# Kernel tuning notes

Measured on AMD Instinct MI355X. Metric: run time of the kernel, lower is better.

## Reference

```python
import jax, jax.numpy as jnp
import numpy as np

N_NODES = 50000
N_EDGES = 800000
IN_DIM = 4
HID = 64
N_LAYERS = 3
BN_EPS = 1e-5


def setup_inputs() -> dict:
    key = jax.random.key(0)
    ks = jax.random.split(key, 16)
    x = jax.random.normal(ks[0], (N_NODES, IN_DIM), dtype=jnp.float32)
    edge_index = jax.random.randint(ks[1], (2, N_EDGES), 0, N_NODES, dtype=jnp.int32)
    # input projection
    W_in = jax.random.normal(ks[2], (IN_DIM, HID), dtype=jnp.float32) * 0.1
    b_in = jnp.zeros((HID,), dtype=jnp.float32)
    # stacked per-layer GCN weights and BatchNorm (eval-mode) params
    conv_w = jax.random.normal(ks[3], (N_LAYERS, HID, HID), dtype=jnp.float32) * 0.1
    conv_b = jnp.zeros((N_LAYERS, HID), dtype=jnp.float32)
    bn_gamma = jnp.ones((N_LAYERS, HID), dtype=jnp.float32)
    bn_beta = jnp.zeros((N_LAYERS, HID), dtype=jnp.float32)
    bn_mean = jax.random.normal(ks[4], (N_LAYERS, HID), dtype=jnp.float32) * 0.01
    bn_var = jnp.abs(jax.random.normal(ks[5], (N_LAYERS, HID), dtype=jnp.float32)) * 0.1 + 1.0
    # output projection: Linear(HID,HID) -> ReLU -> Dropout(eval: identity) -> Linear(HID,OUT)
    W1 = jax.random.normal(ks[6], (HID, HID), dtype=jnp.float32) * 0.1
    b1 = jnp.zeros((HID,), dtype=jnp.float32)
    W2 = jax.random.normal(ks[7], (HID, IN_DIM), dtype=jnp.float32) * 0.01  # xavier gain 0.1
    b2 = jnp.zeros((IN_DIM,), dtype=jnp.float32)
    return {
        "x": x, "edge_index": edge_index,
        "W_in": W_in, "b_in": b_in,
        "conv_w": conv_w, "conv_b": conv_b,
        "bn_gamma": bn_gamma, "bn_beta": bn_beta,
        "bn_mean": bn_mean, "bn_var": bn_var,
        "W1": W1, "b1": b1, "W2": W2, "b2": b2,
    }


def _gcn_graph(edge_index, n_nodes):
    """Add self loops and compute symmetric GCN normalization per edge."""
    loops = jnp.arange(n_nodes, dtype=edge_index.dtype)
    src = jnp.concatenate([edge_index[0], loops])
    dst = jnp.concatenate([edge_index[1], loops])
    deg = jax.ops.segment_sum(jnp.ones_like(dst, dtype=jnp.float32), dst,
                              num_segments=n_nodes)  # in-degree incl. self loop
    dinv = jax.lax.rsqrt(jnp.maximum(deg, 1e-12))
    enorm = dinv[src] * dinv[dst]  # [E+N]
    return src, dst, enorm


def reference(x, edge_index, W_in, b_in, conv_w, conv_b, bn_gamma, bn_beta,
              bn_mean, bn_var, W1, b1, W2, b2):
    n = x.shape[0]
    src, dst, enorm = _gcn_graph(edge_index, n)

    input_x = x
    h = x @ W_in + b_in  # [N, HID]
    for i in range(N_LAYERS):
        residual = h
        # GCNConv: linear -> normalized gather/scatter aggregate -> bias
        hw = h @ conv_w[i]
        msg = hw[src] * enorm[:, None]  # [E+N, HID] irregular gather
        h = jax.ops.segment_sum(msg, dst, num_segments=n) + conv_b[i]
        # BatchNorm1d (eval) + ReLU (dropout is identity in eval)
        h = (h - bn_mean[i]) * jax.lax.rsqrt(bn_var[i] + BN_EPS) * bn_gamma[i] + bn_beta[i]
        h = jax.nn.relu(h)
        h = h + residual  # shapes always match (HID == HID)
    # output projection MLP
    delta = jax.nn.relu(h @ W1 + b1) @ W2 + b2  # [N, IN_DIM]
    return input_x + delta
```

## Files before the change

### kernel.cpp

```cpp
#include <hip/hip_runtime.h>

#define HID 64
#define CAP 64

__device__ __forceinline__ float bf2f(unsigned short u) {
    return __uint_as_float(((unsigned)u) << 16);
}
__device__ __forceinline__ unsigned short f2bf(float f) {
    unsigned u = __float_as_uint(f);
    u += 0x7FFF + ((u >> 16) & 1);
    return (unsigned short)(u >> 16);
}

__global__ void fill_gemm(const int* __restrict__ eidx, int* __restrict__ cursor,
                          int* __restrict__ col, int E, int n, int nodes_per,
                          int chunk, int fillBlocks,
                          const float* __restrict__ x, const float* __restrict__ Win,
                          const float* __restrict__ bin, const float* __restrict__ W,
                          float* __restrict__ h, unsigned short* __restrict__ hws0) {
    if (blockIdx.x < fillBlocks) {
        int p = blockIdx.x & 7;
        int q = blockIdx.x >> 3;
        const int* __restrict__ dst = eidx + E;
        int lo = p * nodes_per;
        int hi = lo + nodes_per;
        int beg = q * chunk;
        int end = min(beg + chunk, E);
        int vend = beg + ((end - beg) & ~3);
        for (int e = beg + threadIdx.x * 4; e < vend; e += 1024) {
            int4 dv = *(const int4*)&dst[e];
            if (dv.x >= lo && dv.x < hi) {
                int s = eidx[e];
                int pos = atomicAdd(&cursor[dv.x], 1);
                if (pos < CAP) col[(dv.x << 6) + pos] = s;
            }
            if (dv.y >= lo && dv.y < hi) {
                int s = eidx[e + 1];
                int pos = atomicAdd(&cursor[dv.y], 1);
                if (pos < CAP) col[(dv.y << 6) + pos] = s;
            }
            if (dv.z >= lo && dv.z < hi) {
                int s = eidx[e + 2];
                int pos = atomicAdd(&cursor[dv.z], 1);
                if (pos < CAP) col[(dv.z << 6) + pos] = s;
            }
            if (dv.w >= lo && dv.w < hi) {
                int s = eidx[e + 3];
                int pos = atomicAdd(&cursor[dv.w], 1);
                if (pos < CAP) col[(dv.w << 6) + pos] = s;
            }
        }
        for (int e = vend + threadIdx.x; e < end; e += 256) {
            int d = dst[e];
            if (d >= lo && d < hi) {
                int s = eidx[e];
                int pos = atomicAdd(&cursor[d], 1);
                if (pos < CAP) col[(d << 6) + pos] = s;
            }
        }
        return;
    }
    __shared__ float wl[64 * 64];
    __shared__ float winl[256];
    __shared__ float binl[64];
    __shared__ float hl[256];
    int b = blockIdx.x - fillBlocks;
    int tid = threadIdx.x;
#pragma unroll
    for (int i = 0; i < 16; ++i) wl[tid + 256 * i] = W[tid + 256 * i];
    winl[tid] = Win[tid];
    if (tid < 64) binl[tid] = bin[tid];
    int j = tid & 63;
    int w = tid >> 6;
    for (int c = 0; c < 8; ++c) {
        int v = b * 32 + c * 4 + w;
        __syncthreads();
        float hv = 0.f;
        if (v < n) {
            float4 xv = *(const float4*)&x[(size_t)v * 4];
            hv = binl[j] + xv.x * winl[j] + xv.y * winl[64 + j]
                         + xv.z * winl[128 + j] + xv.w * winl[192 + j];
            h[(size_t)v * 64 + j] = hv;
        }
        hl[tid] = hv;
        __syncthreads();
        if (v < n) {
            const float* hr = &hl[w * 64];
            float acc = 0.f;
#pragma unroll
            for (int k = 0; k < 64; ++k) acc += hr[k] * wl[k * 64 + j];
            hws0[(size_t)v * 64 + j] = f2bf(acc);
        }
    }
}

#define GATHER_BODY_D(hws4, col, cur, beg, end, s0, s1, s2, s3, gl)               \
    {                                                                             \
        int e = beg;                                                              \
        for (; e + 7 < end; e += 8) {                                             \
            int c0 = col[e], c1 = col[e+1], c2 = col[e+2], c3 = col[e+3];         \
            int c4 = col[e+4], c5 = col[e+5], c6 = col[e+6], c7 = col[e+7];       \
            float d0 = rsqrtf((float)cur[c0] + 1.0f);                             \
            float d1 = rsqrtf((float)cur[c1] + 1.0f);                             \
            float d2 = rsqrtf((float)cur[c2] + 1.0f);                             \
            float d3 = rsqrtf((float)cur[c3] + 1.0f);                             \
            float d4 = rsqrtf((float)cur[c4] + 1.0f);                             \
            float d5 = rsqrtf((float)cur[c5] + 1.0f);                             \
            float d6 = rsqrtf((float)cur[c6] + 1.0f);                             \
            float d7 = rsqrtf((float)cur[c7] + 1.0f);                             \
            ushort4 m0 = hws4[(size_t)c0 * 16 + gl];                              \
            ushort4 m1 = hws4[(size_t)c1 * 16 + gl];                              \
            ushort4 m2 = hws4[(size_t)c2 * 16 + gl];                              \
            ushort4 m3 = hws4[(size_t)c3 * 16 + gl];                              \
            ushort4 m4 = hws4[(size_t)c4 * 16 + gl];                              \
            ushort4 m5 = hws4[(size_t)c5 * 16 + gl];                              \
            ushort4 m6 = hws4[(size_t)c6 * 16 + gl];                              \
            ushort4 m7 = hws4[(size_t)c7 * 16 + gl];                              \
            s0 = fmaf(bf2f(m0.x), d0, s0); s0 = fmaf(bf2f(m1.x), d1, s0);         \
            s0 = fmaf(bf2f(m2.x), d2, s0); s0 = fmaf(bf2f(m3.x), d3, s0);         \
            s0 = fmaf(bf2f(m4.x), d4, s0); s0 = fmaf(bf2f(m5.x), d5, s0);         \
            s0 = fmaf(bf2f(m6.x), d6, s0); s0 = fmaf(bf2f(m7.x), d7, s0);         \
            s1 = fmaf(bf2f(m0.y), d0, s1); s1 = fmaf(bf2f(m1.y), d1, s1);         \
            s1 = fmaf(bf2f(m2.y), d2, s1); s1 = fmaf(bf2f(m3.y), d3, s1);         \
            s1 = fmaf(bf2f(m4.y), d4, s1); s1 = fmaf(bf2f(m5.y), d5, s1);         \
            s1 = fmaf(bf2f(m6.y), d6, s1); s1 = fmaf(bf2f(m7.y), d7, s1);         \
            s2 = fmaf(bf2f(m0.z), d0, s2); s2 = fmaf(bf2f(m1.z), d1, s2);         \
            s2 = fmaf(bf2f(m2.z), d2, s2); s2 = fmaf(bf2f(m3.z), d3, s2);         \
            s2 = fmaf(bf2f(m4.z), d4, s2); s2 = fmaf(bf2f(m5.z), d5, s2);         \
            s2 = fmaf(bf2f(m6.z), d6, s2); s2 = fmaf(bf2f(m7.z), d7, s2);         \
            s3 = fmaf(bf2f(m0.w), d0, s3); s3 = fmaf(bf2f(m1.w), d1, s3);         \
            s3 = fmaf(bf2f(m2.w), d2, s3); s3 = fmaf(bf2f(m3.w), d3, s3);         \
            s3 = fmaf(bf2f(m4.w), d4, s3); s3 = fmaf(bf2f(m5.w), d5, s3);         \
            s3 = fmaf(bf2f(m6.w), d6, s3); s3 = fmaf(bf2f(m7.w), d7, s3);         \
        }                                                                         \
        for (; e < end; ++e) {                                                    \
            int c0 = col[e];                                                      \
            float d0 = rsqrtf((float)cur[c0] + 1.0f);                             \
            ushort4 me = hws4[(size_t)c0 * 16 + gl];                              \
            s0 = fmaf(bf2f(me.x), d0, s0); s1 = fmaf(bf2f(me.y), d0, s1);         \
            s2 = fmaf(bf2f(me.z), d0, s2); s3 = fmaf(bf2f(me.w), d0, s3);         \
        }                                                                         \
    }

#define GATHER_BODY_P(hws4, col, beg, end, s0, s1, s2, s3, gl)                    \
    {                                                                             \
        int e = beg;                                                              \
        for (; e + 7 < end; e += 8) {                                             \
            int c0 = col[e], c1 = col[e+1], c2 = col[e+2], c3 = col[e+3];         \
            int c4 = col[e+4], c5 = col[e+5], c6 = col[e+6], c7 = col[e+7];       \
            ushort4 m0 = hws4[(size_t)c0 * 16 + gl];                              \
            ushort4 m1 = hws4[(size_t)c1 * 16 + gl];                              \
            ushort4 m2 = hws4[(size_t)c2 * 16 + gl];                              \
            ushort4 m3 = hws4[(size_t)c3 * 16 + gl];                              \
            ushort4 m4 = hws4[(size_t)c4 * 16 + gl];                              \
            ushort4 m5 = hws4[(size_t)c5 * 16 + gl];                              \
            ushort4 m6 = hws4[(size_t)c6 * 16 + gl];                              \
            ushort4 m7 = hws4[(size_t)c7 * 16 + gl];                              \
            s0 += bf2f(m0.x)+bf2f(m1.x)+bf2f(m2.x)+bf2f(m3.x)                     \
                + bf2f(m4.x)+bf2f(m5.x)+bf2f(m6.x)+bf2f(m7.x);                    \
            s1 += bf2f(m0.y)+bf2f(m1.y)+bf2f(m2.y)+bf2f(m3.y)                     \
                + bf2f(m4.y)+bf2f(m5.y)+bf2f(m6.y)+bf2f(m7.y);                    \
            s2 += bf2f(m0.z)+bf2f(m1.z)+bf2f(m2.z)+bf2f(m3.z)                     \
                + bf2f(m4.z)+bf2f(m5.z)+bf2f(m6.z)+bf2f(m7.z);                    \
            s3 += bf2f(m0.w)+bf2f(m1.w)+bf2f(m2.w)+bf2f(m3.w)                     \
                + bf2f(m4.w)+bf2f(m5.w)+bf2f(m6.w)+bf2f(m7.w);                    \
        }                                                                         \
        for (; e + 3 < end; e += 4) {                                             \
            int c0 = col[e], c1 = col[e+1], c2 = col[e+2], c3 = col[e+3];         \
            ushort4 m0 = hws4[(size_t)c0 * 16 + gl];                              \
            ushort4 m1 = hws4[(size_t)c1 * 16 + gl];                              \
            ushort4 m2 = hws4[(size_t)c2 * 16 + gl];                              \
            ushort4 m3 = hws4[(size_t)c3 * 16 + gl];                              \
            s0 += bf2f(m0.x)+bf2f(m1.x)+bf2f(m2.x)+bf2f(m3.x);                    \
            s1 += bf2f(m0.y)+bf2f(m1.y)+bf2f(m2.y)+bf2f(m3.y);                    \
            s2 += bf2f(m0.z)+bf2f(m1.z)+bf2f(m2.z)+bf2f(m3.z);                    \
            s3 += bf2f(m0.w)+bf2f(m1.w)+bf2f(m2.w)+bf2f(m3.w);                    \
        }                                                                         \
        for (; e < end; ++e) {                                                    \
            ushort4 me = hws4[(size_t)col[e] * 16 + gl];                          \
            s0 += bf2f(me.x); s1 += bf2f(me.y); s2 += bf2f(me.z); s3 += bf2f(me.w);\
        }                                                                         \
    }

template <bool PRESCALED>
__global__ void gather_gemm(const int* __restrict__ cursor, const int* __restrict__ col,
                            const unsigned short* __restrict__ hws_in,
                            float* __restrict__ h,
                            const float* __restrict__ cb, const float* __restrict__ gamma,
                            const float* __restrict__ beta, const float* __restrict__ mean,
                            const float* __restrict__ var, const float* __restrict__ Wn,
                            unsigned short* __restrict__ hws_out, int n) {
    __shared__ float wl[64 * 64];
    __shared__ float hl[16 * 64];
    int tid = threadIdx.x;
#pragma unroll
    for (int i = 0; i < 16; ++i) wl[tid + 256 * i] = Wn[tid + 256 * i];
    int lane = tid & 63, wave = tid >> 6;
    int grp = lane >> 4, gl = lane & 15;
    int ln = wave * 4 + grp;
    int v = blockIdx.x * 16 + ln;
    bool valid = v < n;
    int vv = valid ? v : 0;
    int j0 = gl * 4;
    const ushort4* hws4 = (const ushort4*)hws_in;
    int cnt = cursor[vv];
    float di = rsqrtf((float)cnt + 1.0f);
    ushort4 m = hws4[(size_t)vv * 16 + gl];
    float s0, s1, s2, s3;
    if (PRESCALED) {
        s0 = bf2f(m.x); s1 = bf2f(m.y); s2 = bf2f(m.z); s3 = bf2f(m.w);
    } else {
        s0 = bf2f(m.x) * di; s1 = bf2f(m.y) * di;
        s2 = bf2f(m.z) * di; s3 = bf2f(m.w) * di;
    }
    int beg = vv << 6;
    int end = beg + (valid ? min(cnt, CAP) : 0);
    if (PRESCALED) {
        GATHER_BODY_P(hws4, col, beg, end, s0, s1, s2, s3, gl)
    } else {
        GATHER_BODY_D(hws4, col, cursor, beg, end, s0, s1, s2, s3, gl)
    }
    float4 cbv = *(const float4*)&cb[j0];
    float4 mnv = *(const float4*)&mean[j0];
    float4 vrv = *(const float4*)&var[j0];
    float4 gmv = *(const float4*)&gamma[j0];
    float4 btv = *(const float4*)&beta[j0];
    float4 hres = *(const float4*)&h[(size_t)vv * 64 + j0];
    float4 o;
    o.x = fmaxf((s0 * di + cbv.x - mnv.x) * rsqrtf(vrv.x + 1e-5f) * gmv.x + btv.x, 0.f) + hres.x;
    o.y = fmaxf((s1 * di + cbv.y - mnv.y) * rsqrtf(vrv.y + 1e-5f) * gmv.y + btv.y, 0.f) + hres.y;
    o.z = fmaxf((s2 * di + cbv.z - mnv.z) * rsqrtf(vrv.z + 1e-5f) * gmv.z + btv.z, 0.f) + hres.z;
    o.w = fmaxf((s3 * di + cbv.w - mnv.w) * rsqrtf(vrv.w + 1e-5f) * gmv.w + btv.w, 0.f) + hres.w;
    if (valid) *(float4*)&h[(size_t)vv * 64 + j0] = o;
    *(float4*)&hl[ln * 64 + j0] = o;
    __syncthreads();
    int j = lane;
    for (int c = 0; c < 4; ++c) {
        int ln2 = wave * 4 + c;
        int v2 = blockIdx.x * 16 + ln2;
        if (v2 < n) {
            const float* hr = &hl[ln2 * 64];
            float acc = 0.f;
#pragma unroll
            for (int k = 0; k < 64; ++k) acc += hr[k] * wl[k * 64 + j];
            float di2 = rsqrtf((float)cursor[v2] + 1.0f);
            hws_out[(size_t)v2 * 64 + j] = f2bf(acc * di2);
        }
    }
}

__global__ void gather_mlp(const int* __restrict__ cursor, const int* __restrict__ col,
                           const unsigned short* __restrict__ hws_in,
                           const float* __restrict__ h,
                           const float* __restrict__ cb, const float* __restrict__ gamma,
                           const float* __restrict__ beta, const float* __restrict__ mean,
                           const float* __restrict__ var, const float* __restrict__ x,
                           const float* __restrict__ W1, const float* __restrict__ b1,
                           const float* __restrict__ W2, const float* __restrict__ b2,
                           float* __restrict__ out, int n) {
    __shared__ float wl[64 * 64];
    __shared__ float w2l[256];
    __shared__ float hl[16 * 64];
    __shared__ float tl[16 * 68];
    int tid = threadIdx.x;
#pragma unroll
    for (int i = 0; i < 16; ++i) wl[tid + 256 * i] = W1[tid + 256 * i];
    w2l[tid] = W2[tid];
    int lane = tid & 63, wave = tid >> 6;
    int grp = lane >> 4, gl = lane & 15;
    int ln = wave * 4 + grp;
    int v = blockIdx.x * 16 + ln;
    bool valid = v < n;
    int vv = valid ? v : 0;
    int j0 = gl * 4;
    const ushort4* hws4 = (const ushort4*)hws_in;
    int cnt = cursor[vv];
    float di = rsqrtf((float)cnt + 1.0f);
    ushort4 m = hws4[(size_t)vv * 16 + gl];
    float s0 = bf2f(m.x), s1 = bf2f(m.y), s2 = bf2f(m.z), s3 = bf2f(m.w);
    int beg = vv << 6;
    int end = beg + (valid ? min(cnt, CAP) : 0);
    GATHER_BODY_P(hws4, col, beg, end, s0, s1, s2, s3, gl)
    float4 cbv = *(const float4*)&cb[j0];
    float4 mnv = *(const float4*)&mean[j0];
    float4 vrv = *(const float4*)&var[j0];
    float4 gmv = *(const float4*)&gamma[j0];
    float4 btv = *(const float4*)&beta[j0];
    float4 hres = *(const float4*)&h[(size_t)vv * 64 + j0];
    float4 o;
    o.x = fmaxf((s0 * di + cbv.x - mnv.x) * rsqrtf(vrv.x + 1e-5f) * gmv.x + btv.x, 0.f) + hres.x;
    o.y = fmaxf((s1 * di + cbv.y - mnv.y) * rsqrtf(vrv.y + 1e-5f) * gmv.y + btv.y, 0.f) + hres.y;
    o.z = fmaxf((s2 * di + cbv.z - mnv.z) * rsqrtf(vrv.z + 1e-5f) * gmv.z + btv.z, 0.f) + hres.z;
    o.w = fmaxf((s3 * di + cbv.w - mnv.w) * rsqrtf(vrv.w + 1e-5f) * gmv.w + btv.w, 0.f) + hres.w;
    *(float4*)&hl[ln * 64 + j0] = o;
    __syncthreads();
    int j = lane;
    float b1j = b1[j];
    for (int c = 0; c < 4; ++c) {
        int ln2 = wave * 4 + c;
        const float* hr = &hl[ln2 * 64];
        float acc = b1j;
#pragma unroll
        for (int k = 0; k < 64; ++k) acc += hr[k] * wl[k * 64 + j];
        tl[ln2 * 68 + j] = fmaxf(acc, 0.f);
    }
    __syncthreads();
    if (tid < 64) {
        int ln2 = tid >> 2, mm = tid & 3;
        int v2 = blockIdx.x * 16 + ln2;
        if (v2 < n) {
            const float* tr = &tl[ln2 * 68];
            float acc = b2[mm];
#pragma unroll
            for (int k = 0; k < 64; ++k) acc += tr[k] * w2l[k * 4 + mm];
            out[(size_t)v2 * 4 + mm] = x[(size_t)v2 * 4 + mm] + acc;
        }
    }
}

extern "C" void kernel_launch(void* const* d_in, const int* in_sizes, int n_in,
                              void* d_out, int out_size, void* d_ws, size_t ws_size,
                              hipStream_t stream) {
    const float* x     = (const float*)d_in[0];
    const int*   eidx  = (const int*)  d_in[1];
    const float* Win   = (const float*)d_in[2];
    const float* bin   = (const float*)d_in[3];
    const float* convw = (const float*)d_in[4];
    const float* convb = (const float*)d_in[5];
    const float* gamma = (const float*)d_in[6];
    const float* beta  = (const float*)d_in[7];
    const float* mean  = (const float*)d_in[8];
    const float* var   = (const float*)d_in[9];
    const float* W1    = (const float*)d_in[10];
    const float* b1    = (const float*)d_in[11];
    const float* W2    = (const float*)d_in[12];
    const float* b2    = (const float*)d_in[13];
    float* out = (float*)d_out;

    int n = in_sizes[0] / 4;
    int E = in_sizes[1] / 2;
    const int B = 256;

    char* p = (char*)d_ws;
    size_t nh = (size_t)n * 64;
    float*          h      = (float*)p;          p += nh * 4;
    unsigned short* hws0   = (unsigned short*)p; p += nh * 2;
    unsigned short* hws1   = (unsigned short*)p; p += nh * 2;
    int*            cursor = (int*)p;            p += ((size_t)n + 16) * 4;
    int*            col    = (int*)p;            p += (size_t)n * CAP * 4;

    const int GP = 128;
    int fillBlocks = GP * 8;
    int nodes_per = (n + 7) / 8;
    int chunk = (((E + GP - 1) / GP) + 3) & ~3;

    hipMemsetAsync(cursor, 0, (size_t)n * 4, stream);
    int NB32 = (n + 31) / 32;
    fill_gemm<<<fillBlocks + NB32, B, 0, stream>>>(
        eidx, cursor, col, E, n, nodes_per, chunk, fillBlocks,
        x, Win, bin, convw, h, hws0);

    int NB16 = (n + 15) / 16;
    gather_gemm<false><<<NB16, B, 0, stream>>>(cursor, col, hws0, h,
        convb, gamma, beta, mean, var, convw + 4096, hws1, n);
    gather_gemm<true><<<NB16, B, 0, stream>>>(cursor, col, hws1, h,
        convb + 64, gamma + 64, beta + 64, mean + 64, var + 64, convw + 8192, hws0, n);
    gather_mlp<<<NB16, B, 0, stream>>>(cursor, col, hws0, h,
        convb + 128, gamma + 128, beta + 128, mean + 128, var + 128,
        x, W1, b1, W2, b2, out, n);
}
```

Baseline: 235.8 us.

## Split feature gathers into two 32-column halves for L2-resident working sets

The bf16 per-node feature table is stored as two separate 32-column half arrays. Each layer's gather runs as two passes: one kernel gathers the first half into an fp32 scratch buffer, and a second gathers the other half and then applies the epilogue and GEMM. Each pass touches a table half the size, about 3.2MB, so it is meant to fit in cache and cut random-access DRAM traffic. In exchange it adds three kernel launches, reads the col index lists twice per layer, and writes and reads an extra fp32 scratch buffer.

```diff
diff --git a/kernel.cpp b/kernel.cpp
--- a/kernel.cpp
+++ b/kernel.cpp
@@ -1,6 +1,5 @@
 #include <hip/hip_runtime.h>
 
-#define HID 64
 #define CAP 64
 
 __device__ __forceinline__ float bf2f(unsigned short u) {
@@ -17,7 +16,8 @@
                           int chunk, int fillBlocks,
                           const float* __restrict__ x, const float* __restrict__ Win,
                           const float* __restrict__ bin, const float* __restrict__ W,
-                          float* __restrict__ h, unsigned short* __restrict__ hws0) {
+                          float* __restrict__ h, unsigned short* __restrict__ hwsA0,
+                          unsigned short* __restrict__ hwsB0) {
     if (blockIdx.x < fillBlocks) {
         int p = blockIdx.x & 7;
         int q = blockIdx.x >> 3;
@@ -89,12 +89,14 @@
             float acc = 0.f;
 #pragma unroll
             for (int k = 0; k < 64; ++k) acc += hr[k] * wl[k * 64 + j];
-            hws0[(size_t)v * 64 + j] = f2bf(acc);
-        }
-    }
-}
-
-#define GATHER_BODY_D(hws4, col, cur, beg, end, s0, s1, s2, s3, gl)               \
+            unsigned short bb = f2bf(acc);
+            if (j < 32) hwsA0[(size_t)v * 32 + j] = bb;
+            else        hwsB0[(size_t)v * 32 + (j - 32)] = bb;
+        }
+    }
+}
+
+#define GH_D(hws2, col, cur, beg, end, s0, s1, gl)                                \
     {                                                                             \
         int e = beg;                                                              \
         for (; e + 7 < end; e += 8) {                                             \
@@ -108,14 +110,14 @@
             float d5 = rsqrtf((float)cur[c5] + 1.0f);                             \
             float d6 = rsqrtf((float)cur[c6] + 1.0f);                             \
             float d7 = rsqrtf((float)cur[c7] + 1.0f);                             \
-            ushort4 m0 = hws4[(size_t)c0 * 16 + gl];                              \
-            ushort4 m1 = hws4[(size_t)c1 * 16 + gl];                              \
-            ushort4 m2 = hws4[(size_t)c2 * 16 + gl];                              \
-            ushort4 m3 = hws4[(size_t)c3 * 16 + gl];                              \
-            ushort4 m4 = hws4[(size_t)c4 * 16 + gl];                              \
-            ushort4 m5 = hws4[(size_t)c5 * 16 + gl];                              \
-            ushort4 m6 = hws4[(size_t)c6 * 16 + gl];                              \
-            ushort4 m7 = hws4[(size_t)c7 * 16 + gl];                              \
+            ushort2 m0 = hws2[(size_t)c0 * 16 + gl];                              \
+            ushort2 m1 = hws2[(size_t)c1 * 16 + gl];                              \
+            ushort2 m2 = hws2[(size_t)c2 * 16 + gl];                              \
+            ushort2 m3 = hws2[(size_t)c3 * 16 + gl];                              \
+            ushort2 m4 = hws2[(size_t)c4 * 16 + gl];                              \
+            ushort2 m5 = hws2[(size_t)c5 * 16 + gl];                              \
+            ushort2 m6 = hws2[(size_t)c6 * 16 + gl];                              \
+            ushort2 m7 = hws2[(size_t)c7 * 16 + gl];                              \
             s0 = fmaf(bf2f(m0.x), d0, s0); s0 = fmaf(bf2f(m1.x), d1, s0);         \
             s0 = fmaf(bf2f(m2.x), d2, s0); s0 = fmaf(bf2f(m3.x), d3, s0);         \
             s0 = fmaf(bf2f(m4.x), d4, s0); s0 = fmaf(bf2f(m5.x), d5, s0);         \
@@ -124,72 +126,81 @@
             s1 = fmaf(bf2f(m2.y), d2, s1); s1 = fmaf(bf2f(m3.y), d3, s1);         \
             s1 = fmaf(bf2f(m4.y), d4, s1); s1 = fmaf(bf2f(m5.y), d5, s1);         \
             s1 = fmaf(bf2f(m6.y), d6, s1); s1 = fmaf(bf2f(m7.y), d7, s1);         \
-            s2 = fmaf(bf2f(m0.z), d0, s2); s2 = fmaf(bf2f(m1.z), d1, s2);         \
-            s2 = fmaf(bf2f(m2.z), d2, s2); s2 = fmaf(bf2f(m3.z), d3, s2);         \
-            s2 = fmaf(bf2f(m4.z), d4, s2); s2 = fmaf(bf2f(m5.z), d5, s2);         \
-            s2 = fmaf(bf2f(m6.z), d6, s2); s2 = fmaf(bf2f(m7.z), d7, s2);         \
-            s3 = fmaf(bf2f(m0.w), d0, s3); s3 = fmaf(bf2f(m1.w), d1, s3);         \
-            s3 = fmaf(bf2f(m2.w), d2, s3); s3 = fmaf(bf2f(m3.w), d3, s3);         \
-            s3 = fmaf(bf2f(m4.w), d4, s3); s3 = fmaf(bf2f(m5.w), d5, s3);         \
-            s3 = fmaf(bf2f(m6.w), d6, s3); s3 = fmaf(bf2f(m7.w), d7, s3);         \
         }                                                                         \
         for (; e < end; ++e) {                                                    \
             int c0 = col[e];                                                      \
             float d0 = rsqrtf((float)cur[c0] + 1.0f);                             \
-            ushort4 me = hws4[(size_t)c0 * 16 + gl];                              \
+            ushort2 me = hws2[(size_t)c0 * 16 + gl];                              \
             s0 = fmaf(bf2f(me.x), d0, s0); s1 = fmaf(bf2f(me.y), d0, s1);         \
-            s2 = fmaf(bf2f(me.z), d0, s2); s3 = fmaf(bf2f(me.w), d0, s3);         \
         }                                                                         \
     }
 
-#define GATHER_BODY_P(hws4, col, beg, end, s0, s1, s2, s3, gl)                    \
+#define GH_P(hws2, col, beg, end, s0, s1, gl)                                     \
     {                                                                             \
         int e = beg;                                                              \
         for (; e + 7 < end; e += 8) {                                             \
             int c0 = col[e], c1 = col[e+1], c2 = col[e+2], c3 = col[e+3];         \
             int c4 = col[e+4], c5 = col[e+5], c6 = col[e+6], c7 = col[e+7];       \
-            ushort4 m0 = hws4[(size_t)c0 * 16 + gl];                              \
-            ushort4 m1 = hws4[(size_t)c1 * 16 + gl];                              \
-            ushort4 m2 = hws4[(size_t)c2 * 16 + gl];                              \
-            ushort4 m3 = hws4[(size_t)c3 * 16 + gl];                              \
-            ushort4 m4 = hws4[(size_t)c4 * 16 + gl];                              \
-            ushort4 m5 = hws4[(size_t)c5 * 16 + gl];                              \
-            ushort4 m6 = hws4[(size_t)c6 * 16 + gl];                              \
-            ushort4 m7 = hws4[(size_t)c7 * 16 + gl];                              \
+            ushort2 m0 = hws2[(size_t)c0 * 16 + gl];                              \
+            ushort2 m1 = hws2[(size_t)c1 * 16 + gl];                              \
+            ushort2 m2 = hws2[(size_t)c2 * 16 + gl];                              \
+            ushort2 m3 = hws2[(size_t)c3 * 16 + gl];                              \
+            ushort2 m4 = hws2[(size_t)c4 * 16 + gl];                              \
+            ushort2 m5 = hws2[(size_t)c5 * 16 + gl];                              \
+            ushort2 m6 = hws2[(size_t)c6 * 16 + gl];                              \
+            ushort2 m7 = hws2[(size_t)c7 * 16 + gl];                              \
             s0 += bf2f(m0.x)+bf2f(m1.x)+bf2f(m2.x)+bf2f(m3.x)                     \
                 + bf2f(m4.x)+bf2f(m5.x)+bf2f(m6.x)+bf2f(m7.x);                    \
             s1 += bf2f(m0.y)+bf2f(m1.y)+bf2f(m2.y)+bf2f(m3.y)                     \
                 + bf2f(m4.y)+bf2f(m5.y)+bf2f(m6.y)+bf2f(m7.y);                    \
-            s2 += bf2f(m0.z)+bf2f(m1.z)+bf2f(m2.z)+bf2f(m3.z)                     \
-                + bf2f(m4.z)+bf2f(m5.z)+bf2f(m6.z)+bf2f(m7.z);                    \
-            s3 += bf2f(m0.w)+bf2f(m1.w)+bf2f(m2.w)+bf2f(m3.w)                     \
-                + bf2f(m4.w)+bf2f(m5.w)+bf2f(m6.w)+bf2f(m7.w);                    \
-        }                                                                         \
-        for (; e + 3 < end; e += 4) {                                             \
-            int c0 = col[e], c1 = col[e+1], c2 = col[e+2], c3 = col[e+3];         \
-            ushort4 m0 = hws4[(size_t)c0 * 16 + gl];                              \
-            ushort4 m1 = hws4[(size_t)c1 * 16 + gl];                              \
-            ushort4 m2 = hws4[(size_t)c2 * 16 + gl];                              \
-            ushort4 m3 = hws4[(size_t)c3 * 16 + gl];                              \
-            s0 += bf2f(m0.x)+bf2f(m1.x)+bf2f(m2.x)+bf2f(m3.x);                    \
-            s1 += bf2f(m0.y)+bf2f(m1.y)+bf2f(m2.y)+bf2f(m3.y);                    \
-            s2 += bf2f(m0.z)+bf2f(m1.z)+bf2f(m2.z)+bf2f(m3.z);                    \
-            s3 += bf2f(m0.w)+bf2f(m1.w)+bf2f(m2.w)+bf2f(m3.w);                    \
         }                                                                         \
         for (; e < end; ++e) {                                                    \
-            ushort4 me = hws4[(size_t)col[e] * 16 + gl];                          \
-            s0 += bf2f(me.x); s1 += bf2f(me.y); s2 += bf2f(me.z); s3 += bf2f(me.w);\
+            ushort2 me = hws2[(size_t)col[e] * 16 + gl];                          \
+            s0 += bf2f(me.x); s1 += bf2f(me.y);                                   \
         }                                                                         \
     }
 
 template <bool PRESCALED>
-__global__ void gather_gemm(const int* __restrict__ cursor, const int* __restrict__ col,
-                            const unsigned short* __restrict__ hws_in,
-                            float* __restrict__ h,
-                            const float* __restrict__ cb, const float* __restrict__ gamma,
-                            const float* __restrict__ beta, const float* __restrict__ mean,
-                            const float* __restrict__ var, const float* __restrict__ Wn,
-                            unsigned short* __restrict__ hws_out, int n) {
+__global__ void gather_half(const int* __restrict__ cursor, const int* __restrict__ col,
+                            const unsigned short* __restrict__ hwsA_in,
+                            float* __restrict__ sA, int n) {
+    int tid = threadIdx.x;
+    int lane = tid & 63, wave = tid >> 6;
+    int grp = lane >> 4, gl = lane & 15;
+    int ln = wave * 4 + grp;
+    int v = blockIdx.x * 16 + ln;
+    bool valid = v < n;
+    int vv = valid ? v : 0;
+    const ushort2* hws2 = (const ushort2*)hwsA_in;
+    int cnt = cursor[vv];
+    ushort2 m = hws2[(size_t)vv * 16 + gl];
+    float s0, s1;
+    if (PRESCALED) {
+        s0 = bf2f(m.x); s1 = bf2f(m.y);
+    } else {
+        float di = rsqrtf((float)cnt + 1.0f);
+        s0 = bf2f(m.x) * di; s1 = bf2f(m.y) * di;
+    }
+    int beg = vv << 6;
+    int end = beg + (valid ? min(cnt, CAP) : 0);
+    if (PRESCALED) {
+        GH_P(hws2, col, beg, end, s0, s1, gl)
+    } else {
+        GH_D(hws2, col, cursor, beg, end, s0, s1, gl)
+    }
+    if (valid) *(float2*)&sA[(size_t)vv * 32 + gl * 2] = make_float2(s0, s1);
+}
+
+template <bool PRESCALED>
+__global__ void gather_gemmB(const int* __restrict__ cursor, const int* __restrict__ col,
+                             const unsigned short* __restrict__ hwsB_in,
+                             const float* __restrict__ sA,
+                             float* __restrict__ h,
+                             const float* __restrict__ cb, const float* __restrict__ gamma,
+                             const float* __restrict__ beta, const float* __restrict__ mean,
+                             const float* __restrict__ var, const float* __restrict__ Wn,
+                             unsigned short* __restrict__ hwsA_out,
+                             unsigned short* __restrict__ hwsB_out, int n) {
     __shared__ float wl[64 * 64];
     __shared__ float hl[16 * 64];
     int tid = threadIdx.x;
@@ -201,38 +212,43 @@
     int v = blockIdx.x * 16 + ln;
     bool valid = v < n;
     int vv = valid ? v : 0;
-    int j0 = gl * 4;
-    const ushort4* hws4 = (const ushort4*)hws_in;
+    const ushort2* hws2 = (const ushort2*)hwsB_in;
     int cnt = cursor[vv];
     float di = rsqrtf((float)cnt + 1.0f);
-    ushort4 m = hws4[(size_t)vv * 16 + gl];
-    float s0, s1, s2, s3;
+    ushort2 m = hws2[(size_t)vv * 16 + gl];
+    float s0, s1;
     if (PRESCALED) {
-        s0 = bf2f(m.x); s1 = bf2f(m.y); s2 = bf2f(m.z); s3 = bf2f(m.w);
+        s0 = bf2f(m.x); s1 = bf2f(m.y);
     } else {
         s0 = bf2f(m.x) * di; s1 = bf2f(m.y) * di;
-        s2 = bf2f(m.z) * di; s3 = bf2f(m.w) * di;
     }
     int beg = vv << 6;
     int end = beg + (valid ? min(cnt, CAP) : 0);
     if (PRESCALED) {
-        GATHER_BODY_P(hws4, col, beg, end, s0, s1, s2, s3, gl)
+        GH_P(hws2, col, beg, end, s0, s1, gl)
     } else {
-        GATHER_BODY_D(hws4, col, cursor, beg, end, s0, s1, s2, s3, gl)
-    }
-    float4 cbv = *(const float4*)&cb[j0];
-    float4 mnv = *(const float4*)&mean[j0];
-    float4 vrv = *(const float4*)&var[j0];
-    float4 gmv = *(const float4*)&gamma[j0];
-    float4 btv = *(const float4*)&beta[j0];
-    float4 hres = *(const float4*)&h[(size_t)vv * 64 + j0];
-    float4 o;
-    o.x = fmaxf((s0 * di + cbv.x - mnv.x) * rsqrtf(vrv.x + 1e-5f) * gmv.x + btv.x, 0.f) + hres.x;
-    o.y = fmaxf((s1 * di + cbv.y - mnv.y) * rsqrtf(vrv.y + 1e-5f) * gmv.y + btv.y, 0.f) + hres.y;
-    o.z = fmaxf((s2 * di + cbv.z - mnv.z) * rsqrtf(vrv.z + 1e-5f) * gmv.z + btv.z, 0.f) + hres.z;
-    o.w = fmaxf((s3 * di + cbv.w - mnv.w) * rsqrtf(vrv.w + 1e-5f) * gmv.w + btv.w, 0.f) + hres.w;
-    if (valid) *(float4*)&h[(size_t)vv * 64 + j0] = o;
-    *(float4*)&hl[ln * 64 + j0] = o;
+        GH_D(hws2, col, cursor, beg, end, s0, s1, gl)
+    }
+    int fa = gl * 2, fb = 32 + gl * 2;
+    float2 a = *(const float2*)&sA[(size_t)vv * 32 + fa];
+    float2 cba = *(const float2*)&cb[fa],   cbb = *(const float2*)&cb[fb];
+    float2 mna = *(const float2*)&mean[fa], mnb = *(const float2*)&mean[fb];
+    float2 vra = *(const float2*)&var[fa],  vrb = *(const float2*)&var[fb];
+    float2 gma = *(const float2*)&gamma[fa], gmb = *(const float2*)&gamma[fb];
+    float2 bta = *(const float2*)&beta[fa], btb = *(const float2*)&beta[fb];
+    float2 ha = *(const float2*)&h[(size_t)vv * 64 + fa];
+    float2 hb = *(const float2*)&h[(size_t)vv * 64 + fb];
+    float2 oa, ob;
+    oa.x = fmaxf((a.x * di + cba.x - mna.x) * rsqrtf(vra.x + 1e-5f) * gma.x + bta.x, 0.f) + ha.x;
+    oa.y = fmaxf((a.y * di + cba.y - mna.y) * rsqrtf(vra.y + 1e-5f) * gma.y + bta.y, 0.f) + ha.y;
+    ob.x = fmaxf((s0 * di + cbb.x - mnb.x) * rsqrtf(vrb.x + 1e-5f) * gmb.x + btb.x, 0.f) + hb.x;
+    ob.y = fmaxf((s1 * di + cbb.y - mnb.y) * rsqrtf(vrb.y + 1e-5f) * gmb.y + btb.y, 0.f) + hb.y;
+    if (valid) {
+        *(float2*)&h[(size_t)vv * 64 + fa] = oa;
+        *(float2*)&h[(size_t)vv * 64 + fb] = ob;
+    }
+    *(float2*)&hl[ln * 64 + fa] = oa;
+    *(float2*)&hl[ln * 64 + fb] = ob;
     __syncthreads();
     int j = lane;
     for (int c = 0; c < 4; ++c) {
@@ -244,20 +260,23 @@
 #pragma unroll
             for (int k = 0; k < 64; ++k) acc += hr[k] * wl[k * 64 + j];
             float di2 = rsqrtf((float)cursor[v2] + 1.0f);
-            hws_out[(size_t)v2 * 64 + j] = f2bf(acc * di2);
-        }
-    }
-}
-
-__global__ void gather_mlp(const int* __restrict__ cursor, const int* __restrict__ col,
-                           const unsigned short* __restrict__ hws_in,
-                           const float* __restrict__ h,
-                           const float* __restrict__ cb, const float* __restrict__ gamma,
-                           const float* __restrict__ beta, const float* __restrict__ mean,
-                           const float* __restrict__ var, const float* __restrict__ x,
-                           const float* __restrict__ W1, const float* __restrict__ b1,
-                           const float* __restrict__ W2, const float* __restrict__ b2,
-                           float* __restrict__ out, int n) {
+            unsigned short bb = f2bf(acc * di2);
+            if (j < 32) hwsA_out[(size_t)v2 * 32 + j] = bb;
+            else        hwsB_out[(size_t)v2 * 32 + (j - 32)] = bb;
+        }
+    }
+}
+
+__global__ void gather_mlpB(const int* __restrict__ cursor, const int* __restrict__ col,
+                            const unsigned short* __restrict__ hwsB_in,
+                            const float* __restrict__ sA,
+                            const float* __restrict__ h,
+                            const float* __restrict__ cb, const float* __restrict__ gamma,
+                            const float* __restrict__ beta, const float* __restrict__ mean,
+                            const float* __restrict__ var, const float* __restrict__ x,
+                            const float* __restrict__ W1, const float* __restrict__ b1,
+                            const float* __restrict__ W2, const float* __restrict__ b2,
+                            float* __restrict__ out, int n) {
     __shared__ float wl[64 * 64];
     __shared__ float w2l[256];
     __shared__ float hl[16 * 64];
@@ -272,27 +291,30 @@
     int v = blockIdx.x * 16 + ln;
     bool valid = v < n;
     int vv = valid ? v : 0;
-    int j0 = gl * 4;
-    const ushort4* hws4 = (const ushort4*)hws_in;
+    const ushort2* hws2 = (const ushort2*)hwsB_in;
     int cnt = cursor[vv];
     float di = rsqrtf((float)cnt + 1.0f);
-    ushort4 m = hws4[(size_t)vv * 16 + gl];
-    float s0 = bf2f(m.x), s1 = bf2f(m.y), s2 = bf2f(m.z), s3 = bf2f(m.w);
+    ushort2 m = hws2[(size_t)vv * 16 + gl];
+    float s0 = bf2f(m.x), s1 = bf2f(m.y);
     int beg = vv << 6;
     int end = beg + (valid ? min(cnt, CAP) : 0);
-    GATHER_BODY_P(hws4, col, beg, end, s0, s1, s2, s3, gl)
-    float4 cbv = *(const float4*)&cb[j0];
-    float4 mnv = *(const float4*)&mean[j0];
-    float4 vrv = *(const float4*)&var[j0];
-    float4 gmv = *(const float4*)&gamma[j0];
-    float4 btv = *(const float4*)&beta[j0];
-    float4 hres = *(const float4*)&h[(size_t)vv * 64 + j0];
-    float4 o;
-    o.x = fmaxf((s0 * di + cbv.x - mnv.x) * rsqrtf(vrv.x + 1e-5f) * gmv.x + btv.x, 0.f) + hres.x;
-    o.y = fmaxf((s1 * di + cbv.y - mnv.y) * rsqrtf(vrv.y + 1e-5f) * gmv.y + btv.y, 0.f) + hres.y;
-    o.z = fmaxf((s2 * di + cbv.z - mnv.z) * rsqrtf(vrv.z + 1e-5f) * gmv.z + btv.z, 0.f) + hres.z;
-    o.w = fmaxf((s3 * di + cbv.w - mnv.w) * rsqrtf(vrv.w + 1e-5f) * gmv.w + btv.w, 0.f) + hres.w;
-    *(float4*)&hl[ln * 64 + j0] = o;
+    GH_P(hws2, col, beg, end, s0, s1, gl)
+    int fa = gl * 2, fb = 32 + gl * 2;
+    float2 a = *(const float2*)&sA[(size_t)vv * 32 + fa];
+    float2 cba = *(const float2*)&cb[fa],   cbb = *(const float2*)&cb[fb];
+    float2 mna = *(const float2*)&mean[fa], mnb = *(const float2*)&mean[fb];
+    float2 vra = *(const float2*)&var[fa],  vrb = *(const float2*)&var[fb];
+    float2 gma = *(const float2*)&gamma[fa], gmb = *(const float2*)&gamma[fb];
+    float2 bta = *(const float2*)&beta[fa], btb = *(const float2*)&beta[fb];
+    float2 ha = *(const float2*)&h[(size_t)vv * 64 + fa];
+    float2 hb = *(const float2*)&h[(size_t)vv * 64 + fb];
+    float2 oa, ob;
+    oa.x = fmaxf((a.x * di + cba.x - mna.x) * rsqrtf(vra.x + 1e-5f) * gma.x + bta.x, 0.f) + ha.x;
+    oa.y = fmaxf((a.y * di + cba.y - mna.y) * rsqrtf(vra.y + 1e-5f) * gma.y + bta.y, 0.f) + ha.y;
+    ob.x = fmaxf((s0 * di + cbb.x - mnb.x) * rsqrtf(vrb.x + 1e-5f) * gmb.x + btb.x, 0.f) + hb.x;
+    ob.y = fmaxf((s1 * di + cbb.y - mnb.y) * rsqrtf(vrb.y + 1e-5f) * gmb.y + btb.y, 0.f) + hb.y;
+    *(float2*)&hl[ln * 64 + fa] = oa;
+    *(float2*)&hl[ln * 64 + fb] = ob;
     __syncthreads();
     int j = lane;
     float b1j = b1[j];
@@ -343,9 +365,13 @@
 
     char* p = (char*)d_ws;
     size_t nh = (size_t)n * 64;
+    size_t nhalf = (size_t)n * 32;
     float*          h      = (float*)p;          p += nh * 4;
-    unsigned short* hws0   = (unsigned short*)p; p += nh * 2;
-    unsigned short* hws1   = (unsigned short*)p; p += nh * 2;
+    unsigned short* hwsA0  = (unsigned short*)p; p += nhalf * 2;
+    unsigned short* hwsB0  = (unsigned short*)p; p += nhalf * 2;
+    unsigned short* hwsA1  = (unsigned short*)p; p += nhalf * 2;
+    unsigned short* hwsB1  = (unsigned short*)p; p += nhalf * 2;
+    float*          sA     = (float*)p;          p += nhalf * 4;
     int*            cursor = (int*)p;            p += ((size_t)n + 16) * 4;
     int*            col    = (int*)p;            p += (size_t)n * CAP * 4;
 
@@ -358,14 +384,17 @@
     int NB32 = (n + 31) / 32;
     fill_gemm<<<fillBlocks + NB32, B, 0, stream>>>(
         eidx, cursor, col, E, n, nodes_per, chunk, fillBlocks,
-        x, Win, bin, convw, h, hws0);
+        x, Win, bin, convw, h, hwsA0, hwsB0);
 
     int NB16 = (n + 15) / 16;
-    gather_gemm<false><<<NB16, B, 0, stream>>>(cursor, col, hws0, h,
-        convb, gamma, beta, mean, var, convw + 4096, hws1, n);
-    gather_gemm<true><<<NB16, B, 0, stream>>>(cursor, col, hws1, h,
-        convb + 64, gamma + 64, beta + 64, mean + 64, var + 64, convw + 8192, hws0, n);
-    gather_mlp<<<NB16, B, 0, stream>>>(cursor, col, hws0, h,
+    gather_half<false><<<NB16, B, 0, stream>>>(cursor, col, hwsA0, sA, n);
+    gather_gemmB<false><<<NB16, B, 0, stream>>>(cursor, col, hwsB0, sA, h,
+        convb, gamma, beta, mean, var, convw + 4096, hwsA1, hwsB1, n);
+    gather_half<true><<<NB16, B, 0, stream>>>(cursor, col, hwsA1, sA, n);
+    gather_gemmB<true><<<NB16, B, 0, stream>>>(cursor, col, hwsB1, sA, h,
+        convb + 64, gamma + 64, beta + 64, mean + 64, var + 64, convw + 8192, hwsA0, hwsB0, n);
+    gather_half<true><<<NB16, B, 0, stream>>>(cursor, col, hwsA0, sA, n);
+    gather_mlpB<<<NB16, B, 0, stream>>>(cursor, col, hwsB0, sA, h,
         convb + 128, gamma + 128, beta + 128, mean + 128, var + 128,
         x, W1, b1, W2, b2, out, n);
 }
```

Result: slower. 276.7 us (+17.4%).
